# Optimization experiments

Measured on AMD Instinct MI355X. Metric: run time of the kernel, lower is better.

Reference implementation:

```python
import jax, jax.numpy as jnp
import numpy as np

B, T, IN, H = 256, 512, 19, 512  # batch, seq_len, input_size, hidden_size
OUT = 1


def setup_inputs() -> dict:
    key = jax.random.key(0)
    ks = jax.random.split(key, 16)
    std = 1.0 / np.sqrt(H)  # reset_parameters: uniform(-1/sqrt(H), 1/sqrt(H))
    u = lambda k, shape: jax.random.uniform(k, shape, jnp.float32, -std, std)
    return {
        "input": jax.random.normal(ks[0], (B, T, IN), jnp.float32),
        "l1_Wx": u(ks[1], (4 * H, IN)),
        "l1_bx": u(ks[2], (4 * H,)),
        "l1_Wh": u(ks[3], (4 * H, H)),
        "l1_bh": u(ks[4], (4 * H,)),
        "l2_Wx": u(ks[5], (4 * H, H)),
        "l2_bx": u(ks[6], (4 * H,)),
        "l2_Wh": u(ks[7], (4 * H, H)),
        "l2_bh": u(ks[8], (4 * H,)),
        "fc1_W": u(ks[9], (H // 2, H)),
        "fc1_b": u(ks[10], (H // 2,)),
        "fc2_W": u(ks[11], (H // 4, H // 2)),
        "fc2_b": u(ks[12], (H // 4,)),
        "fc3_W": u(ks[13], (OUT, H // 4)),
        "fc3_b": u(ks[14], (OUT,)),
    }


def _lstm_layer(x, Wx, bx, Wh, bh):
    # Precompute the input projection for all timesteps (identical math to
    # per-step xh(input), but one big GEMM). x: [B, T, in] -> pre: [B, T, 4H]
    pre = jnp.einsum('bti,gi->btg', x, Wx) + bx
    h_dim = Wh.shape[1]

    def step(carry, p_t):
        h, c = carry
        gates = p_t + h @ Wh.T + bh  # [B, 4H]
        i, f, g, o = jnp.split(gates, 4, axis=-1)
        c = jax.nn.sigmoid(f) * c + jax.nn.sigmoid(i) * jnp.tanh(g)
        h = jax.nn.sigmoid(o) * jnp.tanh(c)
        return (h, c), h

    h0 = jnp.zeros((x.shape[0], h_dim), x.dtype)
    _, hs = jax.lax.scan(step, (h0, h0), jnp.swapaxes(pre, 0, 1))  # hs: [T, B, H]
    return jnp.swapaxes(hs, 0, 1)  # [B, T, H]


def reference(input, l1_Wx, l1_bx, l1_Wh, l1_bh, l2_Wx, l2_bx, l2_Wh, l2_bh,
              fc1_W, fc1_b, fc2_W, fc2_b, fc3_W, fc3_b):
    h1 = _lstm_layer(input, l1_Wx, l1_bx, l1_Wh, l1_bh)
    h2 = _lstm_layer(h1, l2_Wx, l2_bx, l2_Wh, l2_bh)
    out = h2[:, -1, :]  # last timestep of top layer
    out = jax.nn.relu(out @ fc1_W.T + fc1_b)  # dropout = identity (inference)
    out = jax.nn.relu(out @ fc2_W.T + fc2_b)
    out = out @ fc3_W.T + fc3_b
    return jnp.squeeze(out)  # [B]
```

## Files before the change

### kernel.cpp

```cpp
#include <hip/hip_runtime.h>
#include <hip/hip_cooperative_groups.h>

namespace cg = cooperative_groups;

#define Bb   256
#define Tt   512
#define INx  19
#define Hh   512
#define NWG  256
#define NTHR 512

#define WROWS 48
#define WSTR  528
#define WLDS_FLOATS (WROWS * WSTR)
#define WX1_FLOATS  (16 * 20)
#define FCB_FLOATS  (Hh + 256 + 128)
#define SMEM_FLOATS (WLDS_FLOATS + WX1_FLOATS + FCB_FLOATS)
#define SMEM_BYTES  (SMEM_FLOATS * 4)

typedef unsigned int u32;
typedef unsigned long long u64;

__device__ __forceinline__ float sigf(float x) { return 1.0f / (1.0f + __expf(-x)); }
__device__ __forceinline__ float tanhfast(float x) {
    float e = __expf(2.0f * x);
    return 1.0f - 2.0f / (e + 1.0f);
}

union pcast { u64 u; float2 f; };
__device__ __forceinline__ void gstore2(float2* p, float2 v) {
    pcast c; c.f = v;
    __hip_atomic_store((u64*)p, c.u, __ATOMIC_RELAXED, __HIP_MEMORY_SCOPE_AGENT);
}

__device__ __forceinline__ void gbar(u32* flags, int wgid, int tid, u32 phase) {
    __syncthreads();
    if (tid == 0)
        __hip_atomic_store(&flags[wgid], phase, __ATOMIC_RELEASE, __HIP_MEMORY_SCOPE_AGENT);
    if (tid < NWG) {
        const u32* fp = &flags[tid];
        while (__hip_atomic_load(fp, __ATOMIC_RELAXED, __HIP_MEMORY_SCOPE_AGENT) < phase)
            __builtin_amdgcn_s_sleep(2);
    }
    __syncthreads();
    __builtin_amdgcn_fence(__ATOMIC_ACQUIRE, "agent");
}

__device__ __forceinline__ void ldh(const float4* __restrict__ hp, int c,
                                    float4 (&A)[4], float4 (&B)[4]) {
    #pragma unroll
    for (int kk = 0; kk < 4; ++kk) {
        A[kk] = hp[(size_t)(c * 4 + kk) * 128];
        B[kk] = hp[(size_t)(c * 4 + kk) * 128 + 1];
    }
}

__device__ __forceinline__ void fmac(const float4 (&A)[4], const float4 (&B)[4],
                                     const float* __restrict__ wk,
                                     float (&a1)[4][4], float (&a2)[4][4]) {
    #pragma unroll
    for (int g = 0; g < 4; ++g) {
        const float4 w1 = *reinterpret_cast<const float4*>(wk + (0 + g) * WSTR);
        const float4 w2 = *reinterpret_cast<const float4*>(wk + (4 + g) * WSTR);
        const float4 w3 = *reinterpret_cast<const float4*>(wk + (8 + g) * WSTR);
        a1[g][0] += A[0].x*w1.x + A[1].x*w1.y + A[2].x*w1.z + A[3].x*w1.w;
        a1[g][1] += A[0].z*w1.x + A[1].z*w1.y + A[2].z*w1.z + A[3].z*w1.w;
        a1[g][2] += B[0].x*w1.x + B[1].x*w1.y + B[2].x*w1.z + B[3].x*w1.w;
        a1[g][3] += B[0].z*w1.x + B[1].z*w1.y + B[2].z*w1.z + B[3].z*w1.w;
        a2[g][0] += A[0].x*w2.x + A[1].x*w2.y + A[2].x*w2.z + A[3].x*w2.w
                  + A[0].y*w3.x + A[1].y*w3.y + A[2].y*w3.z + A[3].y*w3.w;
        a2[g][1] += A[0].z*w2.x + A[1].z*w2.y + A[2].z*w2.z + A[3].z*w2.w
                  + A[0].w*w3.x + A[1].w*w3.y + A[2].w*w3.z + A[3].w*w3.w;
        a2[g][2] += B[0].x*w2.x + B[1].x*w2.y + B[2].x*w2.z + B[3].x*w2.w
                  + B[0].y*w3.x + B[1].y*w3.y + B[2].y*w3.z + B[3].y*w3.w;
        a2[g][3] += B[0].z*w2.x + B[1].z*w2.y + B[2].z*w2.z + B[3].z*w2.w
                  + B[0].w*w3.x + B[1].w*w3.y + B[2].w*w3.z + B[3].w*w3.w;
    }
}

__global__ void __launch_bounds__(NTHR, 2)
lstm_fused(const float* __restrict__ input,
           const float* __restrict__ l1_Wx, const float* __restrict__ l1_bx,
           const float* __restrict__ l1_Wh, const float* __restrict__ l1_bh,
           const float* __restrict__ l2_Wx, const float* __restrict__ l2_bx,
           const float* __restrict__ l2_Wh, const float* __restrict__ l2_bh,
           const float* __restrict__ fc1_W, const float* __restrict__ fc1_b,
           const float* __restrict__ fc2_W, const float* __restrict__ fc2_b,
           const float* __restrict__ fc3_W, const float* __restrict__ fc3_b,
           float* __restrict__ out, float* __restrict__ ws)
{
    extern __shared__ float smem[];
    float* wlds = smem;
    float* wx1l = smem + WLDS_FLOATS;
    float* fcb  = wx1l + WX1_FLOATS;

    cg::grid_group grid = cg::this_grid();
    const int wgid = blockIdx.x;
    const int ug = wgid >> 1;
    const int bs = wgid & 1;
    const int jb = ug * 4;
    const int tid = threadIdx.x;

    const int wid = __builtin_amdgcn_readfirstlane(tid >> 6);
    const int su = wid & 3;
    const int bh = wid >> 2;
    const int lane = tid & 63;
    const int kq = lane >> 4;
    const int bg = lane & 15;
    const int bB = bs * 128 + bh * 64 + bg * 4;
    const int j  = jb + su;

    float2* PA = (float2*)ws;
    float2* PB = PA + (size_t)Hh * Bb;
    u32* flags = (u32*)(PB + (size_t)Hh * Bb);

    if (tid == 0)
        __hip_atomic_store(&flags[wgid], 0u, __ATOMIC_RELAXED, __HIP_MEMORY_SCOPE_AGENT);
    grid.sync();

    for (int idx = tid; idx < WROWS * Hh; idx += NTHR) {
        const int row = idx >> 9, k = idx & 511;
        const int u = row / 12, rr = row - u * 12;
        const int m = rr >> 2, g = rr & 3;
        const float* src = (m == 0) ? l1_Wh : (m == 1) ? l2_Wx : l2_Wh;
        wlds[row * WSTR + (k >> 7) * 132 + (k & 127)] =
            src[(size_t)(g * Hh + jb + u) * Hh + k];
    }
    if (tid < 16 * INx) {
        const int r = tid / INx, i = tid - r * INx;
        const int u = r >> 2, g = r & 3;
        wx1l[r * 20 + i] = l1_Wx[(size_t)(g * Hh + jb + u) * INx + i];
    }
    float b1r[4], b2r[4];
    #pragma unroll
    for (int g = 0; g < 4; ++g) {
        const int row = g * Hh + j;
        b1r[g] = l1_bx[row] + l1_bh[row];
        b2r[g] = l2_bx[row] + l2_bh[row];
    }
    __syncthreads();

    const float* wlane = wlds + (su * 12) * WSTR + kq * 132;

    float c1[4] = {0.f, 0.f, 0.f, 0.f}, c2[4] = {0.f, 0.f, 0.f, 0.f};
    if (kq == 0) {
        #pragma unroll
        for (int b = 0; b < 4; ++b) {
            const float* xr = input + (size_t)(bB + b) * Tt * INx;
            float s[4];
            #pragma unroll
            for (int g = 0; g < 4; ++g) {
                float acc = b1r[g];
                #pragma unroll
                for (int i = 0; i < INx; ++i) acc += xr[i] * wx1l[(su * 4 + g) * 20 + i];
                s[g] = acc;
            }
            c1[b] = sigf(s[0]) * tanhfast(s[2]);
            gstore2(&PA[(size_t)j * Bb + bB + b],
                    make_float2(sigf(s[3]) * tanhfast(c1[b]), 0.f));
        }
    }
    gbar(flags, wgid, tid, 1u);

    const float2* Pc = PA; float2* Pn = PB;

    for (int t = 0; t < Tt; ++t) {
        const bool doL1 = (t < Tt - 1);

        float a1[4][4], a2[4][4];
        #pragma unroll
        for (int g = 0; g < 4; ++g)
            #pragma unroll
            for (int b = 0; b < 4; ++b) { a1[g][b] = 0.f; a2[g][b] = 0.f; }

        const float4* hp = (const float4*)Pc + (size_t)(kq * 128) * 128 + (bB >> 1);

        float4 Ac[4], Bc[4], An[4], Bn[4];
        ldh(hp, 0, Ac, Bc);
        #pragma unroll 1
        for (int c = 0; c < 32; c += 2) {
            ldh(hp, c + 1, An, Bn);
            fmac(Ac, Bc, wlane + (c    ) * 4, a1, a2);
            if (c < 30) ldh(hp, c + 2, Ac, Bc);
            fmac(An, Bn, wlane + (c + 1) * 4, a1, a2);
        }

        #pragma unroll
        for (int g = 0; g < 4; ++g) {
            #pragma unroll
            for (int b = 0; b < 4; ++b) {
                float v = a1[g][b]; v += __shfl_xor(v, 16, 64); v += __shfl_xor(v, 32, 64); a1[g][b] = v;
                float w = a2[g][b]; w += __shfl_xor(w, 16, 64); w += __shfl_xor(w, 32, 64); a2[g][b] = w;
            }
        }

        if (kq == 0) {
            #pragma unroll
            for (int b = 0; b < 4; ++b) {
                const int bb = bB + b;
                float h1v = 0.f;
                if (doL1) {
                    const float* xr = input + ((size_t)bb * Tt + t + 1) * INx;
                    float s1[4];
                    #pragma unroll
                    for (int g = 0; g < 4; ++g) {
                        float acc = a1[g][b] + b1r[g];
                        #pragma unroll
                        for (int i = 0; i < INx; ++i) acc += xr[i] * wx1l[(su * 4 + g) * 20 + i];
                        s1[g] = acc;
                    }
                    const float ig = sigf(s1[0]), fg = sigf(s1[1]);
                    const float gg = tanhfast(s1[2]), og = sigf(s1[3]);
                    c1[b] = fg * c1[b] + ig * gg;
                    h1v = og * tanhfast(c1[b]);
                }
                const float ig = sigf(a2[0][b] + b2r[0]);
                const float fg = sigf(a2[1][b] + b2r[1]);
                const float gg = tanhfast(a2[2][b] + b2r[2]);
                const float og = sigf(a2[3][b] + b2r[3]);
                c2[b] = fg * c2[b] + ig * gg;
                gstore2(&Pn[(size_t)j * Bb + bb], make_float2(h1v, og * tanhfast(c2[b])));
            }
        }

        gbar(flags, wgid, tid, (u32)(t + 2));

        const float2* tp = Pc; Pc = Pn; Pn = (float2*)tp;
    }

    float* hh  = fcb;
    float* a1s = fcb + Hh;
    float* a2s = fcb + Hh + 256;
    hh[tid] = Pc[(size_t)tid * Bb + wgid].y;
    __syncthreads();
    if (tid < 256) {
        float acc = fc1_b[tid];
        const float* wr = fc1_W + (size_t)tid * Hh;
        for (int i = 0; i < Hh; ++i) acc += wr[i] * hh[i];
        a1s[tid] = fmaxf(acc, 0.0f);
    }
    __syncthreads();
    if (tid < 128) {
        float acc = fc2_b[tid];
        const float* wr = fc2_W + (size_t)tid * 256;
        for (int i = 0; i < 256; ++i) acc += wr[i] * a1s[i];
        a2s[tid] = fmaxf(acc, 0.0f);
    }
    __syncthreads();
    if (tid == 0) {
        float acc = fc3_b[0];
        for (int i = 0; i < 128; ++i) acc += fc3_W[i] * a2s[i];
        out[wgid] = acc;
    }
}

extern "C" void kernel_launch(void* const* d_in, const int* in_sizes, int n_in,
                              void* d_out, int out_size, void* d_ws, size_t ws_size,
                              hipStream_t stream)
{
    (void)in_sizes; (void)n_in; (void)out_size; (void)ws_size;

    const float* input = (const float*)d_in[0];
    const float* l1_Wx = (const float*)d_in[1];
    const float* l1_bx = (const float*)d_in[2];
    const float* l1_Wh = (const float*)d_in[3];
    const float* l1_bh = (const float*)d_in[4];
    const float* l2_Wx = (const float*)d_in[5];
    const float* l2_bx = (const float*)d_in[6];
    const float* l2_Wh = (const float*)d_in[7];
    const float* l2_bh = (const float*)d_in[8];
    const float* fc1_W = (const float*)d_in[9];
    const float* fc1_b = (const float*)d_in[10];
    const float* fc2_W = (const float*)d_in[11];
    const float* fc2_b = (const float*)d_in[12];
    const float* fc3_W = (const float*)d_in[13];
    const float* fc3_b = (const float*)d_in[14];
    float* out = (float*)d_out;
    float* ws  = (float*)d_ws;

    hipFuncSetAttribute((const void*)lstm_fused,
                        hipFuncAttributeMaxDynamicSharedMemorySize, SMEM_BYTES);

    void* args[] = {
        &input,
        &l1_Wx, &l1_bx, &l1_Wh, &l1_bh,
        &l2_Wx, &l2_bx, &l2_Wh, &l2_bh,
        &fc1_W, &fc1_b, &fc2_W, &fc2_b, &fc3_W, &fc3_b,
        &out, &ws
    };
    hipLaunchCooperativeKernel((void*)lstm_fused, dim3(NWG), dim3(NTHR), args,
                               SMEM_BYTES, stream);
}
```

Before: 28.47 ms.

## Replace flag-array grid barrier with atomic counter and spread gate math across lanes

```diff
diff --git a/kernel.cpp b/kernel.cpp
--- a/kernel.cpp
+++ b/kernel.cpp
@@ -32,30 +32,33 @@
     pcast c; c.f = v;
     __hip_atomic_store((u64*)p, c.u, __ATOMIC_RELAXED, __HIP_MEMORY_SCOPE_AGENT);
 }
-
-__device__ __forceinline__ void gbar(u32* flags, int wgid, int tid, u32 phase) {
-    __syncthreads();
-    if (tid == 0)
-        __hip_atomic_store(&flags[wgid], phase, __ATOMIC_RELEASE, __HIP_MEMORY_SCOPE_AGENT);
-    if (tid < NWG) {
-        const u32* fp = &flags[tid];
-        while (__hip_atomic_load(fp, __ATOMIC_RELAXED, __HIP_MEMORY_SCOPE_AGENT) < phase)
+__device__ __forceinline__ float2 gload2(const float2* p) {
+    pcast c;
+    c.u = __hip_atomic_load((const u64*)p, __ATOMIC_RELAXED, __HIP_MEMORY_SCOPE_AGENT);
+    return c.f;
+}
+
+__device__ __forceinline__ void cbar(u32* ctr, int tid, u32 phase) {
+    __syncthreads();
+    if (tid == 0) {
+        __hip_atomic_fetch_add(ctr, 1u, __ATOMIC_RELEASE, __HIP_MEMORY_SCOPE_AGENT);
+        const u32 target = phase * (u32)NWG;
+        while (__hip_atomic_load(ctr, __ATOMIC_RELAXED, __HIP_MEMORY_SCOPE_AGENT) < target)
             __builtin_amdgcn_s_sleep(2);
     }
     __syncthreads();
-    __builtin_amdgcn_fence(__ATOMIC_ACQUIRE, "agent");
-}
-
-__device__ __forceinline__ void ldh(const float4* __restrict__ hp, int c,
-                                    float4 (&A)[4], float4 (&B)[4]) {
+}
+
+__device__ __forceinline__ void ldchunk(const float2* __restrict__ hp, int c,
+                                        float2 (&H)[4][4]) {
     #pragma unroll
-    for (int kk = 0; kk < 4; ++kk) {
-        A[kk] = hp[(size_t)(c * 4 + kk) * 128];
-        B[kk] = hp[(size_t)(c * 4 + kk) * 128 + 1];
-    }
-}
-
-__device__ __forceinline__ void fmac(const float4 (&A)[4], const float4 (&B)[4],
+    for (int kk = 0; kk < 4; ++kk)
+        #pragma unroll
+        for (int b = 0; b < 4; ++b)
+            H[kk][b] = gload2(hp + (size_t)(c * 4 + kk) * Bb + b);
+}
+
+__device__ __forceinline__ void fmac(const float2 (&H)[4][4],
                                      const float* __restrict__ wk,
                                      float (&a1)[4][4], float (&a2)[4][4]) {
     #pragma unroll
@@ -63,19 +66,21 @@
         const float4 w1 = *reinterpret_cast<const float4*>(wk + (0 + g) * WSTR);
         const float4 w2 = *reinterpret_cast<const float4*>(wk + (4 + g) * WSTR);
         const float4 w3 = *reinterpret_cast<const float4*>(wk + (8 + g) * WSTR);
-        a1[g][0] += A[0].x*w1.x + A[1].x*w1.y + A[2].x*w1.z + A[3].x*w1.w;
-        a1[g][1] += A[0].z*w1.x + A[1].z*w1.y + A[2].z*w1.z + A[3].z*w1.w;
-        a1[g][2] += B[0].x*w1.x + B[1].x*w1.y + B[2].x*w1.z + B[3].x*w1.w;
-        a1[g][3] += B[0].z*w1.x + B[1].z*w1.y + B[2].z*w1.z + B[3].z*w1.w;
-        a2[g][0] += A[0].x*w2.x + A[1].x*w2.y + A[2].x*w2.z + A[3].x*w2.w
-                  + A[0].y*w3.x + A[1].y*w3.y + A[2].y*w3.z + A[3].y*w3.w;
-        a2[g][1] += A[0].z*w2.x + A[1].z*w2.y + A[2].z*w2.z + A[3].z*w2.w
-                  + A[0].w*w3.x + A[1].w*w3.y + A[2].w*w3.z + A[3].w*w3.w;
-        a2[g][2] += B[0].x*w2.x + B[1].x*w2.y + B[2].x*w2.z + B[3].x*w2.w
-                  + B[0].y*w3.x + B[1].y*w3.y + B[2].y*w3.z + B[3].y*w3.w;
-        a2[g][3] += B[0].z*w2.x + B[1].z*w2.y + B[2].z*w2.z + B[3].z*w2.w
-                  + B[0].w*w3.x + B[1].w*w3.y + B[2].w*w3.z + B[3].w*w3.w;
-    }
+        #pragma unroll
+        for (int b = 0; b < 4; ++b) {
+            a1[g][b] += H[0][b].x*w1.x + H[1][b].x*w1.y + H[2][b].x*w1.z + H[3][b].x*w1.w;
+            a2[g][b] += H[0][b].x*w2.x + H[1][b].x*w2.y + H[2][b].x*w2.z + H[3][b].x*w2.w
+                      + H[0][b].y*w3.x + H[1][b].y*w3.y + H[2][b].y*w3.z + H[3][b].y*w3.w;
+        }
+    }
+}
+
+__device__ __forceinline__ float sel4(const float (&a)[4], int k) {
+    float v = a[0];
+    v = (k == 1) ? a[1] : v;
+    v = (k == 2) ? a[2] : v;
+    v = (k == 3) ? a[3] : v;
+    return v;
 }
 
 __global__ void __launch_bounds__(NTHR, 2)
@@ -108,14 +113,15 @@
     const int kq = lane >> 4;
     const int bg = lane & 15;
     const int bB = bs * 128 + bh * 64 + bg * 4;
+    const int bfin = bB + kq;
     const int j  = jb + su;
 
     float2* PA = (float2*)ws;
     float2* PB = PA + (size_t)Hh * Bb;
-    u32* flags = (u32*)(PB + (size_t)Hh * Bb);
-
-    if (tid == 0)
-        __hip_atomic_store(&flags[wgid], 0u, __ATOMIC_RELAXED, __HIP_MEMORY_SCOPE_AGENT);
+    u32* ctr = (u32*)(PB + (size_t)Hh * Bb);
+
+    if (wgid == 0 && tid == 0)
+        __hip_atomic_store(ctr, 0u, __ATOMIC_RELAXED, __HIP_MEMORY_SCOPE_AGENT);
     grid.sync();
 
     for (int idx = tid; idx < WROWS * Hh; idx += NTHR) {
@@ -142,25 +148,22 @@
 
     const float* wlane = wlds + (su * 12) * WSTR + kq * 132;
 
-    float c1[4] = {0.f, 0.f, 0.f, 0.f}, c2[4] = {0.f, 0.f, 0.f, 0.f};
-    if (kq == 0) {
-        #pragma unroll
-        for (int b = 0; b < 4; ++b) {
-            const float* xr = input + (size_t)(bB + b) * Tt * INx;
-            float s[4];
+    float c1 = 0.f, c2 = 0.f;
+    {
+        const float* xr = input + (size_t)bfin * Tt * INx;
+        float s[4];
+        #pragma unroll
+        for (int g = 0; g < 4; ++g) {
+            float acc = b1r[g];
             #pragma unroll
-            for (int g = 0; g < 4; ++g) {
-                float acc = b1r[g];
-                #pragma unroll
-                for (int i = 0; i < INx; ++i) acc += xr[i] * wx1l[(su * 4 + g) * 20 + i];
-                s[g] = acc;
-            }
-            c1[b] = sigf(s[0]) * tanhfast(s[2]);
-            gstore2(&PA[(size_t)j * Bb + bB + b],
-                    make_float2(sigf(s[3]) * tanhfast(c1[b]), 0.f));
-        }
-    }
-    gbar(flags, wgid, tid, 1u);
+            for (int i = 0; i < INx; ++i) acc += xr[i] * wx1l[(su * 4 + g) * 20 + i];
+            s[g] = acc;
+        }
+        c1 = sigf(s[0]) * tanhfast(s[2]);
+        gstore2(&PA[(size_t)j * Bb + bfin],
+                make_float2(sigf(s[3]) * tanhfast(c1), 0.f));
+    }
+    cbar(ctr, tid, 1u);
 
     const float2* Pc = PA; float2* Pn = PB;
 
@@ -173,16 +176,16 @@
             #pragma unroll
             for (int b = 0; b < 4; ++b) { a1[g][b] = 0.f; a2[g][b] = 0.f; }
 
-        const float4* hp = (const float4*)Pc + (size_t)(kq * 128) * 128 + (bB >> 1);
-
-        float4 Ac[4], Bc[4], An[4], Bn[4];
-        ldh(hp, 0, Ac, Bc);
+        const float2* hp = Pc + (size_t)(kq * 128) * Bb + bB;
+
+        float2 HA[4][4], HB[4][4];
+        ldchunk(hp, 0, HA);
         #pragma unroll 1
         for (int c = 0; c < 32; c += 2) {
-            ldh(hp, c + 1, An, Bn);
-            fmac(Ac, Bc, wlane + (c    ) * 4, a1, a2);
-            if (c < 30) ldh(hp, c + 2, Ac, Bc);
-            fmac(An, Bn, wlane + (c + 1) * 4, a1, a2);
+            ldchunk(hp, c + 1, HB);
+            fmac(HA, wlane + (c    ) * 4, a1, a2);
+            if (c < 30) ldchunk(hp, c + 2, HA);
+            fmac(HB, wlane + (c + 1) * 4, a1, a2);
         }
 
         #pragma unroll
@@ -194,36 +197,32 @@
             }
         }
 
-        if (kq == 0) {
-            #pragma unroll
-            for (int b = 0; b < 4; ++b) {
-                const int bb = bB + b;
-                float h1v = 0.f;
-                if (doL1) {
-                    const float* xr = input + ((size_t)bb * Tt + t + 1) * INx;
-                    float s1[4];
+        {
+            float h1v = 0.f;
+            if (doL1) {
+                const float* xr = input + ((size_t)bfin * Tt + t + 1) * INx;
+                float s1[4];
+                #pragma unroll
+                for (int g = 0; g < 4; ++g) {
+                    float acc = sel4(a1[g], kq) + b1r[g];
                     #pragma unroll
-                    for (int g = 0; g < 4; ++g) {
-                        float acc = a1[g][b] + b1r[g];
-                        #pragma unroll
-                        for (int i = 0; i < INx; ++i) acc += xr[i] * wx1l[(su * 4 + g) * 20 + i];
-                        s1[g] = acc;
-                    }
-                    const float ig = sigf(s1[0]), fg = sigf(s1[1]);
-                    const float gg = tanhfast(s1[2]), og = sigf(s1[3]);
-                    c1[b] = fg * c1[b] + ig * gg;
-                    h1v = og * tanhfast(c1[b]);
+                    for (int i = 0; i < INx; ++i) acc += xr[i] * wx1l[(su * 4 + g) * 20 + i];
+                    s1[g] = acc;
                 }
-                const float ig = sigf(a2[0][b] + b2r[0]);
-                const float fg = sigf(a2[1][b] + b2r[1]);
-                const float gg = tanhfast(a2[2][b] + b2r[2]);
-                const float og = sigf(a2[3][b] + b2r[3]);
-                c2[b] = fg * c2[b] + ig * gg;
-                gstore2(&Pn[(size_t)j * Bb + bb], make_float2(h1v, og * tanhfast(c2[b])));
+                const float ig = sigf(s1[0]), fg = sigf(s1[1]);
+                const float gg = tanhfast(s1[2]), og = sigf(s1[3]);
+                c1 = fg * c1 + ig * gg;
+                h1v = og * tanhfast(c1);
             }
-        }
-
-        gbar(flags, wgid, tid, (u32)(t + 2));
+            const float ig = sigf(sel4(a2[0], kq) + b2r[0]);
+            const float fg = sigf(sel4(a2[1], kq) + b2r[1]);
+            const float gg = tanhfast(sel4(a2[2], kq) + b2r[2]);
+            const float og = sigf(sel4(a2[3], kq) + b2r[3]);
+            c2 = fg * c2 + ig * gg;
+            gstore2(&Pn[(size_t)j * Bb + bfin], make_float2(h1v, og * tanhfast(c2)));
+        }
+
+        cbar(ctr, tid, (u32)(t + 2));
 
         const float2* tp = Pc; Pc = Pn; Pn = (float2*)tp;
     }
@@ -231,7 +230,7 @@
     float* hh  = fcb;
     float* a1s = fcb + Hh;
     float* a2s = fcb + Hh + 256;
-    hh[tid] = Pc[(size_t)tid * Bb + wgid].y;
+    hh[tid] = gload2(&Pc[(size_t)tid * Bb + wgid]).y;
     __syncthreads();
     if (tid < 256) {
         float acc = fc1_b[tid];
```

New measurement: 88.82 ms. 3.12x slower.
